# Performance work log

Hardware: AMD Instinct MI355X
Metric: run time of the kernel (lower is better)

The kernel has to match this reference:

```python
import jax, jax.numpy as jnp
import numpy as np

N_HEADS = 8
N_POINTS = 4


def _bilinear_sample(vl, g, Hl, Wl):
    # vl: [B, nH, Hl*Wl, hd] level values; g: [B, Q, nH, P, 2] sampling locs in [0,1] (x, y)
    # Emulates torch grid_sample(mode='bilinear', padding_mode='zeros', align_corners=False)
    B, Q, nH, P, _ = g.shape
    hd = vl.shape[-1]
    x = g[..., 0] * Wl - 0.5
    y = g[..., 1] * Hl - 0.5
    x0f = jnp.floor(x)
    y0f = jnp.floor(y)
    x0 = x0f.astype(jnp.int32)
    y0 = y0f.astype(jnp.int32)
    wx1 = x - x0f
    wy1 = y - y0f

    def corner(xi, yi, w):
        valid = (xi >= 0) & (xi < Wl) & (yi >= 0) & (yi < Hl)
        idx = jnp.clip(yi, 0, Hl - 1) * Wl + jnp.clip(xi, 0, Wl - 1)  # [B,Q,nH,P]
        idx = idx.transpose(0, 2, 1, 3).reshape(B, nH, Q * P)
        gathered = jnp.take_along_axis(vl, idx[..., None], axis=2)  # [B,nH,Q*P,hd]
        wm = (w * valid.astype(w.dtype)).transpose(0, 2, 1, 3).reshape(B, nH, Q * P)
        return gathered * wm[..., None]

    s = (corner(x0, y0, (1.0 - wx1) * (1.0 - wy1))
         + corner(x0 + 1, y0, wx1 * (1.0 - wy1))
         + corner(x0, y0 + 1, (1.0 - wx1) * wy1)
         + corner(x0 + 1, y0 + 1, wx1 * wy1))
    return s.reshape(B, nH, Q, P, hd)


def setup_inputs() -> dict:
    key = jax.random.key(0)
    ks = jax.random.split(key, 12)
    B, Q, D = 32, 300, 256
    L, P, nH = 4, N_POINTS, N_HEADS
    shapes = np.array([[80, 80], [40, 40], [20, 20], [10, 10]], dtype=np.int32)
    V = int((shapes[:, 0] * shapes[:, 1]).sum())  # 8500
    lsi = np.concatenate([[0], np.cumsum(shapes[:, 0] * shapes[:, 1])[:-1]]).astype(np.int32)
    sd = 1.0 / np.sqrt(D)
    return {
        'query': jax.random.normal(ks[0], (B, Q, D), jnp.float32),
        'reference_points': jax.random.uniform(ks[1], (B, Q, L, 2), jnp.float32),
        'value': jax.random.normal(ks[2], (B, V, D), jnp.float32),
        'spatial_shapes': jnp.asarray(shapes),
        'level_start_index': jnp.asarray(lsi),
        'W_off': jax.random.normal(ks[3], (D, nH * L * P * 2), jnp.float32) * sd,
        'b_off': jax.random.normal(ks[4], (nH * L * P * 2,), jnp.float32) * 0.5,
        'W_attn': jax.random.normal(ks[5], (D, nH * L * P), jnp.float32) * sd,
        'b_attn': jax.random.normal(ks[6], (nH * L * P,), jnp.float32) * 0.1,
        'W_val': jax.random.normal(ks[7], (D, D), jnp.float32) * sd,
        'b_val': jnp.zeros((D,), jnp.float32),
        'W_out': jax.random.normal(ks[8], (D, D), jnp.float32) * sd,
        'b_out': jnp.zeros((D,), jnp.float32),
    }


def reference(query, reference_points, value, spatial_shapes, level_start_index,
              W_off, b_off, W_attn, b_attn, W_val, b_val, W_out, b_out):
    shapes = np.asarray(spatial_shapes)  # static level shapes
    B, Q, D = query.shape
    nH, P = N_HEADS, N_POINTS
    L = shapes.shape[0]
    hd = D // nH

    val = value @ W_val + b_val  # [B,V,D]
    val = val.reshape(B, -1, nH, hd).transpose(0, 2, 1, 3)  # [B,nH,V,hd]

    off = (query @ W_off + b_off).reshape(B, Q, nH, L, P, 2)
    attn = jax.nn.softmax((query @ W_attn + b_attn).reshape(B, Q, nH, L * P), axis=-1)
    attn = attn.reshape(B, Q, nH, L, P)

    # normalizer is (W_l, H_l)
    norm = jnp.asarray(np.stack([shapes[:, 1], shapes[:, 0]], -1), jnp.float32)  # [L,2]
    loc = reference_points[:, :, None, :, None, :] + off / norm[None, None, None, :, None, :]

    out = jnp.zeros((B, Q, nH, hd), query.dtype)
    start = 0
    for lvl in range(L):
        Hl, Wl = int(shapes[lvl, 0]), int(shapes[lvl, 1])
        vl = val[:, :, start:start + Hl * Wl, :]  # [B,nH,HW,hd]
        sampled = _bilinear_sample(vl, loc[:, :, :, lvl], Hl, Wl)  # [B,nH,Q,P,hd]
        out = out + jnp.einsum('bnqpd,bqnp->bqnd', sampled, attn[:, :, :, lvl])
        start += Hl * Wl

    return out.reshape(B, Q, D) @ W_out + b_out
```

## Files before the change

kernel.cpp:

```cpp
#include <hip/hip_runtime.h>
#include <hip/hip_bf16.h>
#include <math.h>
#include <stdint.h>

#define NB 32
#define NQ 300
#define ND 256
#define NH 8
#define HD 32
#define NL 4
#define NP 4
#define V_TOT 8500
#define BQ_TOT (NB*NQ)
#define MVAL (NB*V_TOT)
#define NOA 384

typedef short v8s __attribute__((ext_vector_type(8)));
typedef float v4f __attribute__((ext_vector_type(4)));

#define AS1 __attribute__((address_space(1)))
#define AS3 __attribute__((address_space(3)))

__device__ __forceinline__ void copy16_async(const void* g, void* l) {
#if __has_builtin(__builtin_amdgcn_global_load_lds)
    __builtin_amdgcn_global_load_lds((const AS1 unsigned int*)g,
                                     (AS3 unsigned int*)l, 16, 0, 0);
#else
    *(uint4*)l = *(const uint4*)g;
#endif
}

__device__ __forceinline__ unsigned short f2bf_rne(float x) {
    unsigned u = __float_as_uint(x);
    u += 0x7fffu + ((u >> 16) & 1u);
    return (unsigned short)(u >> 16);
}
__device__ __forceinline__ float bf2f(unsigned short b) {
    return __uint_as_float(((unsigned)b) << 16);
}

__device__ __forceinline__ void split2(float f0, float f1,
                                       unsigned& hp, unsigned& lp) {
    float2 v; v.x = f0; v.y = f1;
    __hip_bfloat162 h = __float22bfloat162_rn(v);
    unsigned hu; __builtin_memcpy(&hu, &h, 4);
    const float h0 = __uint_as_float(hu << 16);
    const float h1 = __uint_as_float(hu & 0xffff0000u);
    float2 l; l.x = f0 - h0; l.y = f1 - h1;
    __hip_bfloat162 lo = __float22bfloat162_rn(l);
    unsigned lu; __builtin_memcpy(&lu, &lo, 4);
    hp = hu; lp = lu;
}

__device__ __forceinline__ int swz_pos(int n, int k) {
    const int base = k & ~31;
    const int o = (k >> 3) & 3;
    const int op = o ^ ((n >> 1) & 3);
    return n * 256 + base + (op << 3) + (k & 7);
}

__global__ __launch_bounds__(256) void prep_weights(
    const float* __restrict__ W_val, const float* __restrict__ W_off,
    const float* __restrict__ W_attn, const float* __restrict__ W_out,
    const float* __restrict__ b_off, const float* __restrict__ b_attn,
    unsigned short* __restrict__ Bval_h, unsigned short* __restrict__ Bval_l,
    unsigned short* __restrict__ Boa_h,  unsigned short* __restrict__ Boa_l,
    unsigned short* __restrict__ Bout_h, unsigned short* __restrict__ Bout_l,
    float* __restrict__ b_oa)
{
    const int t = blockIdx.x * 256 + threadIdx.x;
    if (t < 65536) {
        const int n = t >> 8, k = t & 255;
        const float x = W_val[k * 256 + n];
        const unsigned short hi = f2bf_rne(x);
        const unsigned short lo = f2bf_rne(x - bf2f(hi));
        const int p = swz_pos(n, k);
        Bval_h[p] = hi; Bval_l[p] = lo;
    } else if (t < 65536 + 98304) {
        const int t2 = t - 65536;
        const int n = t2 >> 8, k = t2 & 255;
        const float x = (n < 256) ? W_off[k * 256 + n] : W_attn[k * 128 + (n - 256)];
        const unsigned short hi = f2bf_rne(x);
        const unsigned short lo = f2bf_rne(x - bf2f(hi));
        const int p = swz_pos(n, k);
        Boa_h[p] = hi; Boa_l[p] = lo;
    } else if (t < 229376) {
        const int t3 = t - 163840;
        const int n = t3 >> 8, k = t3 & 255;
        const float x = W_out[k * 256 + n];
        const unsigned short hi = f2bf_rne(x);
        const unsigned short lo = f2bf_rne(x - bf2f(hi));
        const int p = swz_pos(n, k);
        Bout_h[p] = hi; Bout_l[p] = lo;
    } else {
        const int t4 = t - 229376;
        if (t4 < NOA) b_oa[t4] = (t4 < 256) ? b_off[t4] : b_attn[t4 - 256];
    }
}

__global__ __launch_bounds__(256) void gemm_a32(
    const float* __restrict__ A,
    const unsigned short* __restrict__ Bh,
    const unsigned short* __restrict__ Bl,
    const float* __restrict__ bias,
    float* __restrict__ Cf,
    unsigned short* __restrict__ Cb,
    int ldc, int mode)
{
    __shared__ unsigned short Ah[128][32];
    __shared__ unsigned short Al[128][32];
    __shared__ unsigned short Bs[2][128][32];

    const int tid  = threadIdx.x;
    const int row0 = blockIdx.x * 128;
    const int col0 = blockIdx.y * 128;
    const int wave = tid >> 6;
    const int lane = tid & 63;
    const int wm   = (wave >> 1) * 64;
    const int wn   = (wave & 1) * 64;
    const int m16  = lane & 15;
    const int quad = lane >> 4;

    v4f acc[4][4] = {};

    for (int k0 = 0; k0 < 256; k0 += 32) {
        unsigned hpk[2][4], lpk[2][4];
        int rr[2], oo[2];
#pragma unroll
        for (int i = 0; i < 2; ++i) {
            const int idx = tid + i * 256;
            const int r   = idx >> 2;
            const int o   = idx & 3;
            rr[i] = r;
            oo[i] = (o ^ ((r >> 1) & 3)) << 3;
            const float4 f0 = *(const float4*)(A + (size_t)(row0 + r) * 256 + k0 + o * 8);
            const float4 f1 = *(const float4*)(A + (size_t)(row0 + r) * 256 + k0 + o * 8 + 4);
            split2(f0.x, f0.y, hpk[i][0], lpk[i][0]);
            split2(f0.z, f0.w, hpk[i][1], lpk[i][1]);
            split2(f1.x, f1.y, hpk[i][2], lpk[i][2]);
            split2(f1.z, f1.w, hpk[i][3], lpk[i][3]);
        }

        __syncthreads();

#pragma unroll
        for (int c = 0; c < 2; ++c) {
            const int linear = (wave * 2 + c) * 1024 + lane * 16;
            const int n   = linear >> 6;
            const int off = linear & 63;
            copy16_async((const char*)Bh + ((size_t)(col0 + n) * 256 + k0) * 2 + off,
                         (char*)&Bs[0][0][0] + linear);
            copy16_async((const char*)Bl + ((size_t)(col0 + n) * 256 + k0) * 2 + off,
                         (char*)&Bs[1][0][0] + linear);
        }

#pragma unroll
        for (int i = 0; i < 2; ++i) {
            *(uint4*)&Ah[rr[i]][oo[i]] = make_uint4(hpk[i][0], hpk[i][1], hpk[i][2], hpk[i][3]);
            *(uint4*)&Al[rr[i]][oo[i]] = make_uint4(lpk[i][0], lpk[i][1], lpk[i][2], lpk[i][3]);
        }

        __syncthreads();

        v8s ah[4], al[4], bh[4], bl[4];
#pragma unroll
        for (int i = 0; i < 4; ++i) {
            const int r  = wm + i * 16 + m16;
            const int ka = (quad ^ ((r >> 1) & 3)) << 3;
            ah[i] = *(v8s*)&Ah[r][ka];
            al[i] = *(v8s*)&Al[r][ka];
            const int n  = wn + i * 16 + m16;
            const int ko = (quad ^ ((n >> 1) & 3)) << 3;
            bh[i] = *(v8s*)&Bs[0][n][ko];
            bl[i] = *(v8s*)&Bs[1][n][ko];
        }
#pragma unroll
        for (int i = 0; i < 4; ++i)
#pragma unroll
            for (int j = 0; j < 4; ++j) {
                acc[i][j] = __builtin_amdgcn_mfma_f32_16x16x32_bf16(ah[i], bh[j], acc[i][j], 0, 0, 0);
                acc[i][j] = __builtin_amdgcn_mfma_f32_16x16x32_bf16(ah[i], bl[j], acc[i][j], 0, 0, 0);
                acc[i][j] = __builtin_amdgcn_mfma_f32_16x16x32_bf16(al[i], bh[j], acc[i][j], 0, 0, 0);
            }
    }

#pragma unroll
    for (int j = 0; j < 4; ++j) {
        const int cl = col0 + wn + j * 16 + m16;
        const float bb = bias[cl];
        if (mode == 0) {
#pragma unroll
            for (int i = 0; i < 4; ++i)
#pragma unroll
                for (int r = 0; r < 4; ++r) {
                    const int R = row0 + wm + i * 16 + quad * 4 + r;
                    Cf[(size_t)R * ldc + cl] = acc[i][j][r] + bb;
                }
        } else {
            const int h  = cl >> 5;
            const int dh = cl & 31;
#pragma unroll
            for (int i = 0; i < 4; ++i)
#pragma unroll
                for (int r = 0; r < 4; ++r) {
                    const int R = row0 + wm + i * 16 + quad * 4 + r;
                    const unsigned b = (unsigned)R / V_TOT;
                    const int v = R - (int)b * V_TOT;
                    Cb[(((size_t)(b * NH + h)) * V_TOT + v) * HD + dh] =
                        f2bf_rne(acc[i][j][r] + bb);
                }
        }
    }
}

__global__ __launch_bounds__(256) void gemm_a16(
    const unsigned short* __restrict__ A,
    const unsigned short* __restrict__ Bh,
    const unsigned short* __restrict__ Bl,
    const float* __restrict__ bias,
    float* __restrict__ C, int ldc)
{
    __shared__ unsigned short As[2][128][32];
    __shared__ unsigned short Bs[2][2][128][32];

    const int tid  = threadIdx.x;
    const int row0 = blockIdx.x * 128;
    const int col0 = blockIdx.y * 128;
    const int wave = tid >> 6;
    const int lane = tid & 63;
    const int wm   = (wave >> 1) * 64;
    const int wn   = (wave & 1) * 64;
    const int m16  = lane & 15;
    const int quad = lane >> 4;

    v4f acc[4][4] = {};

#pragma unroll
    for (int c = 0; c < 2; ++c) {
        const int linear = (wave * 2 + c) * 1024 + lane * 16;
        const int n   = linear >> 6;
        const int off = linear & 63;
        copy16_async((const char*)A  + ((size_t)(row0 + n) * 256 + 0) * 2 + off,
                     (char*)&As[0][0][0] + linear);
        copy16_async((const char*)Bh + ((size_t)(col0 + n) * 256 + 0) * 2 + off,
                     (char*)&Bs[0][0][0][0] + linear);
        copy16_async((const char*)Bl + ((size_t)(col0 + n) * 256 + 0) * 2 + off,
                     (char*)&Bs[0][1][0][0] + linear);
    }
    __syncthreads();

    for (int t = 0; t < 8; ++t) {
        const int buf = t & 1;
        const int nb  = buf ^ 1;
        const int k1  = (t + 1) << 5;

        if (t < 7) {
#pragma unroll
            for (int c = 0; c < 2; ++c) {
                const int linear = (wave * 2 + c) * 1024 + lane * 16;
                const int n   = linear >> 6;
                const int off = linear & 63;
                copy16_async((const char*)A  + ((size_t)(row0 + n) * 256 + k1) * 2 + off,
                             (char*)&As[nb][0][0] + linear);
                copy16_async((const char*)Bh + ((size_t)(col0 + n) * 256 + k1) * 2 + off,
                             (char*)&Bs[nb][0][0][0] + linear);
                copy16_async((const char*)Bl + ((size_t)(col0 + n) * 256 + k1) * 2 + off,
                             (char*)&Bs[nb][1][0][0] + linear);
            }
        }

        v8s a[4], bh[4], bl[4];
#pragma unroll
        for (int i = 0; i < 4; ++i) {
            const int r  = wm + i * 16 + m16;
            const int ka = (quad ^ ((r >> 1) & 3)) << 3;
            a[i] = *(v8s*)&As[buf][r][ka];
            const int n  = wn + i * 16 + m16;
            const int kb = (quad ^ ((n >> 1) & 3)) << 3;
            bh[i] = *(v8s*)&Bs[buf][0][n][kb];
            bl[i] = *(v8s*)&Bs[buf][1][n][kb];
        }
#pragma unroll
        for (int i = 0; i < 4; ++i)
#pragma unroll
            for (int j = 0; j < 4; ++j) {
                acc[i][j] = __builtin_amdgcn_mfma_f32_16x16x32_bf16(a[i], bh[j], acc[i][j], 0, 0, 0);
                acc[i][j] = __builtin_amdgcn_mfma_f32_16x16x32_bf16(a[i], bl[j], acc[i][j], 0, 0, 0);
            }

        __syncthreads();
    }

#pragma unroll
    for (int j = 0; j < 4; ++j) {
        const int cl = col0 + wn + j * 16 + m16;
        const float bb = bias[cl];
#pragma unroll
        for (int i = 0; i < 4; ++i)
#pragma unroll
            for (int r = 0; r < 4; ++r) {
                const int R = row0 + wm + i * 16 + quad * 4 + r;
                C[(size_t)R * ldc + cl] = acc[i][j][r] + bb;
            }
    }
}

__global__ __launch_bounds__(256) void sample_kernel(
    const float* __restrict__ refp,
    const float* __restrict__ offattn,
    const unsigned short* __restrict__ val,
    unsigned short* __restrict__ pre)
{
    const int t  = blockIdx.x * 256 + threadIdx.x;
    const int d8 = t & 3;
    const int h  = (t >> 2) & 7;
    const int bq = t >> 5;
    const int b  = bq / NQ;

    const float* rp = refp + (size_t)bq * 8;
    const float* op = offattn + (size_t)bq * 384 + h * 32;
    const float* ap = offattn + (size_t)bq * 384 + 256 + h * 16;

    float aw[16];
    float m = -1e30f;
#pragma unroll
    for (int i = 0; i < 16; ++i) { aw[i] = ap[i]; m = fmaxf(m, aw[i]); }
    float s = 0.f;
#pragma unroll
    for (int i = 0; i < 16; ++i) { aw[i] = __expf(aw[i] - m); s += aw[i]; }
    const float inv = 1.f / s;
#pragma unroll
    for (int i = 0; i < 16; ++i) aw[i] *= inv;

    const int Hs[4] = {80, 40, 20, 10};
    const int St[4] = {0, 6400, 8000, 8400};

    float acc[8] = {};
#pragma unroll
    for (int l = 0; l < NL; ++l) {
        const int Wl = Hs[l], Hl = Hs[l];
        const float fW = (float)Wl, fH = (float)Hl;
        const float rx = rp[l * 2 + 0];
        const float ry = rp[l * 2 + 1];
        const unsigned short* vb =
            val + (((size_t)(b * NH + h)) * V_TOT + St[l]) * HD + d8 * 8;
#pragma unroll
        for (int p = 0; p < NP; ++p) {
            const float ox = op[l * 8 + p * 2 + 0];
            const float oy = op[l * 8 + p * 2 + 1];
            const float w  = aw[l * 4 + p];
            const float x = fmaf(rx, fW, ox) - 0.5f;
            const float y = fmaf(ry, fH, oy) - 0.5f;
            const float x0f = floorf(x), y0f = floorf(y);
            const int   x0 = (int)x0f,  y0 = (int)y0f;
            const float wx1 = x - x0f,  wy1 = y - y0f;
            const float wx0 = 1.f - wx1, wy0 = 1.f - wy1;
#pragma unroll
            for (int cy = 0; cy < 2; ++cy) {
#pragma unroll
                for (int cx = 0; cx < 2; ++cx) {
                    const int xi = x0 + cx;
                    const int yi = y0 + cy;
                    float cw = (cx ? wx1 : wx0) * (cy ? wy1 : wy0) * w;
                    const bool valid = (xi >= 0) && (xi < Wl) && (yi >= 0) && (yi < Hl);
                    cw = valid ? cw : 0.f;
                    const int xc = xi < 0 ? 0 : (xi > Wl - 1 ? Wl - 1 : xi);
                    const int yc = yi < 0 ? 0 : (yi > Hl - 1 ? Hl - 1 : yi);
                    const uint4 g = *(const uint4*)(vb + (size_t)(yc * Wl + xc) * HD);
                    const unsigned gu[4] = {g.x, g.y, g.z, g.w};
#pragma unroll
                    for (int e = 0; e < 4; ++e) {
                        acc[2*e]   = fmaf(cw, __uint_as_float(gu[e] << 16),        acc[2*e]);
                        acc[2*e+1] = fmaf(cw, __uint_as_float(gu[e] & 0xffff0000u), acc[2*e+1]);
                    }
                }
            }
        }
    }

    unsigned o[4];
#pragma unroll
    for (int e = 0; e < 4; ++e)
        o[e] = (unsigned)f2bf_rne(acc[2*e]) | ((unsigned)f2bf_rne(acc[2*e+1]) << 16);
    const int octswz = d8 ^ ((bq >> 1) & 3);
    *(uint4*)(pre + (size_t)bq * 256 + h * 32 + octswz * 8) =
        make_uint4(o[0], o[1], o[2], o[3]);
}

extern "C" void kernel_launch(void* const* d_in, const int* in_sizes, int n_in,
                              void* d_out, int out_size, void* d_ws, size_t ws_size,
                              hipStream_t stream)
{
    const float* query  = (const float*)d_in[0];
    const float* refp   = (const float*)d_in[1];
    const float* value  = (const float*)d_in[2];
    const float* W_off  = (const float*)d_in[5];
    const float* b_off  = (const float*)d_in[6];
    const float* W_attn = (const float*)d_in[7];
    const float* b_attn = (const float*)d_in[8];
    const float* W_val  = (const float*)d_in[9];
    const float* b_val  = (const float*)d_in[10];
    const float* W_out  = (const float*)d_in[11];
    const float* b_out  = (const float*)d_in[12];
    float* out = (float*)d_out;

    char* ws = (char*)d_ws;
    unsigned short* val     = (unsigned short*)ws;
    float*          offattn = (float*)(ws + 139264000);
    unsigned short* pre     = (unsigned short*)(ws + 154009600);
    unsigned short* Bval_h  = (unsigned short*)(ws + 158924800);
    unsigned short* Bval_l  = Bval_h + 65536;
    unsigned short* Boa_h   = Bval_l + 65536;
    unsigned short* Boa_l   = Boa_h + 98304;
    unsigned short* Bout_h  = Boa_l + 98304;
    unsigned short* Bout_l  = Bout_h + 65536;
    float*          b_oa    = (float*)(Bout_l + 65536);

    const dim3 blk(256);

    prep_weights<<<dim3(898), blk, 0, stream>>>(
        W_val, W_off, W_attn, W_out, b_off, b_attn,
        Bval_h, Bval_l, Boa_h, Boa_l, Bout_h, Bout_l, b_oa);

    gemm_a32<<<dim3(MVAL / 128, 2), blk, 0, stream>>>(
        value, Bval_h, Bval_l, b_val, nullptr, val, 0, 1);

    gemm_a32<<<dim3(BQ_TOT / 128, 3), blk, 0, stream>>>(
        query, Boa_h, Boa_l, b_oa, offattn, nullptr, NOA, 0);

    sample_kernel<<<dim3((BQ_TOT * 32) / 256), blk, 0, stream>>>(
        refp, offattn, val, pre);

    gemm_a16<<<dim3(BQ_TOT / 128, 2), blk, 0, stream>>>(
        pre, Bout_h, Bout_l, b_out, out, 256);
}
```

Before: 617.2 us.

## Prefetch A tiles into registers, swap grid axes, add occupancy hint in gemm_a32

Restructures the fp32-input split-bf16 GEMM so the next K-slice of A is loaded into registers while the current slice is split and stored, hiding global load latency. The grid is transposed so the column blocks that share the same A rows run next to each other, which should improve L2 reuse of the large value matrix. B fragments are now loaded inside the j loop to cut live registers, and launch_bounds asks for 3 blocks per SM. The cost is extra registers for the prefetched data and a risk of spills under the tighter occupancy target.

After: 576.2 us. -6.6%, faster.

```diff
diff --git a/kernel.cpp b/kernel.cpp
--- a/kernel.cpp
+++ b/kernel.cpp
@@ -98,7 +98,7 @@
     }
 }
 
-__global__ __launch_bounds__(256) void gemm_a32(
+__global__ __launch_bounds__(256, 3) void gemm_a32(
     const float* __restrict__ A,
     const unsigned short* __restrict__ Bh,
     const unsigned short* __restrict__ Bl,
@@ -112,8 +112,8 @@
     __shared__ unsigned short Bs[2][128][32];
 
     const int tid  = threadIdx.x;
-    const int row0 = blockIdx.x * 128;
-    const int col0 = blockIdx.y * 128;
+    const int col0 = blockIdx.x * 128;
+    const int row0 = blockIdx.y * 128;
     const int wave = tid >> 6;
     const int lane = tid & 63;
     const int wm   = (wave >> 1) * 64;
@@ -121,67 +121,84 @@
     const int m16  = lane & 15;
     const int quad = lane >> 4;
 
+    const int i0  = tid;
+    const int i1  = tid + 256;
+    const int r0_ = i0 >> 2, o0_ = i0 & 3;
+    const int r1_ = i1 >> 2, o1_ = i1 & 3;
+    const int oo0 = (o0_ ^ ((r0_ >> 1) & 3)) << 3;
+    const int oo1 = (o1_ ^ ((r1_ >> 1) & 3)) << 3;
+    const float* Ap0 = A + (size_t)(row0 + r0_) * 256 + o0_ * 8;
+    const float* Ap1 = A + (size_t)(row0 + r1_) * 256 + o1_ * 8;
+
+    const int lin0 = (wave * 2 + 0) * 1024 + lane * 16;
+    const int lin1 = (wave * 2 + 1) * 1024 + lane * 16;
+    const char* pBh0 = (const char*)Bh + ((size_t)(col0 + (lin0 >> 6)) * 256) * 2 + (lin0 & 63);
+    const char* pBl0 = (const char*)Bl + ((size_t)(col0 + (lin0 >> 6)) * 256) * 2 + (lin0 & 63);
+    const char* pBh1 = (const char*)Bh + ((size_t)(col0 + (lin1 >> 6)) * 256) * 2 + (lin1 & 63);
+    const char* pBl1 = (const char*)Bl + ((size_t)(col0 + (lin1 >> 6)) * 256) * 2 + (lin1 & 63);
+    char* lBh0 = (char*)&Bs[0][0][0] + lin0;
+    char* lBh1 = (char*)&Bs[0][0][0] + lin1;
+    char* lBl0 = (char*)&Bs[1][0][0] + lin0;
+    char* lBl1 = (char*)&Bs[1][0][0] + lin1;
+
     v4f acc[4][4] = {};
 
-    for (int k0 = 0; k0 < 256; k0 += 32) {
-        unsigned hpk[2][4], lpk[2][4];
-        int rr[2], oo[2];
-#pragma unroll
-        for (int i = 0; i < 2; ++i) {
-            const int idx = tid + i * 256;
-            const int r   = idx >> 2;
-            const int o   = idx & 3;
-            rr[i] = r;
-            oo[i] = (o ^ ((r >> 1) & 3)) << 3;
-            const float4 f0 = *(const float4*)(A + (size_t)(row0 + r) * 256 + k0 + o * 8);
-            const float4 f1 = *(const float4*)(A + (size_t)(row0 + r) * 256 + k0 + o * 8 + 4);
-            split2(f0.x, f0.y, hpk[i][0], lpk[i][0]);
-            split2(f0.z, f0.w, hpk[i][1], lpk[i][1]);
-            split2(f1.x, f1.y, hpk[i][2], lpk[i][2]);
-            split2(f1.z, f1.w, hpk[i][3], lpk[i][3]);
+    float4 f00 = *(const float4*)(Ap0);
+    float4 f01 = *(const float4*)(Ap0 + 4);
+    float4 f10 = *(const float4*)(Ap1);
+    float4 f11 = *(const float4*)(Ap1 + 4);
+
+#pragma unroll
+    for (int t = 0; t < 8; ++t) {
+        unsigned hpk0[4], lpk0[4], hpk1[4], lpk1[4];
+        split2(f00.x, f00.y, hpk0[0], lpk0[0]);
+        split2(f00.z, f00.w, hpk0[1], lpk0[1]);
+        split2(f01.x, f01.y, hpk0[2], lpk0[2]);
+        split2(f01.z, f01.w, hpk0[3], lpk0[3]);
+        split2(f10.x, f10.y, hpk1[0], lpk1[0]);
+        split2(f10.z, f10.w, hpk1[1], lpk1[1]);
+        split2(f11.x, f11.y, hpk1[2], lpk1[2]);
+        split2(f11.z, f11.w, hpk1[3], lpk1[3]);
+
+        if (t < 7) {
+            const int k1 = (t + 1) * 32;
+            f00 = *(const float4*)(Ap0 + k1);
+            f01 = *(const float4*)(Ap0 + k1 + 4);
+            f10 = *(const float4*)(Ap1 + k1);
+            f11 = *(const float4*)(Ap1 + k1 + 4);
         }
 
         __syncthreads();
 
-#pragma unroll
-        for (int c = 0; c < 2; ++c) {
-            const int linear = (wave * 2 + c) * 1024 + lane * 16;
-            const int n   = linear >> 6;
-            const int off = linear & 63;
-            copy16_async((const char*)Bh + ((size_t)(col0 + n) * 256 + k0) * 2 + off,
-                         (char*)&Bs[0][0][0] + linear);
-            copy16_async((const char*)Bl + ((size_t)(col0 + n) * 256 + k0) * 2 + off,
-                         (char*)&Bs[1][0][0] + linear);
-        }
-
-#pragma unroll
-        for (int i = 0; i < 2; ++i) {
-            *(uint4*)&Ah[rr[i]][oo[i]] = make_uint4(hpk[i][0], hpk[i][1], hpk[i][2], hpk[i][3]);
-            *(uint4*)&Al[rr[i]][oo[i]] = make_uint4(lpk[i][0], lpk[i][1], lpk[i][2], lpk[i][3]);
-        }
+        copy16_async(pBh0 + t * 64, lBh0);
+        copy16_async(pBh1 + t * 64, lBh1);
+        copy16_async(pBl0 + t * 64, lBl0);
+        copy16_async(pBl1 + t * 64, lBl1);
+
+        *(uint4*)&Ah[r0_][oo0] = make_uint4(hpk0[0], hpk0[1], hpk0[2], hpk0[3]);
+        *(uint4*)&Al[r0_][oo0] = make_uint4(lpk0[0], lpk0[1], lpk0[2], lpk0[3]);
+        *(uint4*)&Ah[r1_][oo1] = make_uint4(hpk1[0], hpk1[1], hpk1[2], hpk1[3]);
+        *(uint4*)&Al[r1_][oo1] = make_uint4(lpk1[0], lpk1[1], lpk1[2], lpk1[3]);
 
         __syncthreads();
 
-        v8s ah[4], al[4], bh[4], bl[4];
 #pragma unroll
         for (int i = 0; i < 4; ++i) {
             const int r  = wm + i * 16 + m16;
             const int ka = (quad ^ ((r >> 1) & 3)) << 3;
-            ah[i] = *(v8s*)&Ah[r][ka];
-            al[i] = *(v8s*)&Al[r][ka];
-            const int n  = wn + i * 16 + m16;
-            const int ko = (quad ^ ((n >> 1) & 3)) << 3;
-            bh[i] = *(v8s*)&Bs[0][n][ko];
-            bl[i] = *(v8s*)&Bs[1][n][ko];
-        }
-#pragma unroll
-        for (int i = 0; i < 4; ++i)
+            const v8s ah = *(v8s*)&Ah[r][ka];
+            const v8s al = *(v8s*)&Al[r][ka];
 #pragma unroll
             for (int j = 0; j < 4; ++j) {
-                acc[i][j] = __builtin_amdgcn_mfma_f32_16x16x32_bf16(ah[i], bh[j], acc[i][j], 0, 0, 0);
-                acc[i][j] = __builtin_amdgcn_mfma_f32_16x16x32_bf16(ah[i], bl[j], acc[i][j], 0, 0, 0);
-                acc[i][j] = __builtin_amdgcn_mfma_f32_16x16x32_bf16(al[i], bh[j], acc[i][j], 0, 0, 0);
+                const int n  = wn + j * 16 + m16;
+                const int ko = (quad ^ ((n >> 1) & 3)) << 3;
+                const v8s bh = *(v8s*)&Bs[0][n][ko];
+                const v8s bl = *(v8s*)&Bs[1][n][ko];
+                acc[i][j] = __builtin_amdgcn_mfma_f32_16x16x32_bf16(ah, bh, acc[i][j], 0, 0, 0);
+                acc[i][j] = __builtin_amdgcn_mfma_f32_16x16x32_bf16(ah, bl, acc[i][j], 0, 0, 0);
+                acc[i][j] = __builtin_amdgcn_mfma_f32_16x16x32_bf16(al, bh, acc[i][j], 0, 0, 0);
             }
+        }
     }
 
 #pragma unroll
@@ -422,10 +439,10 @@
         W_val, W_off, W_attn, W_out, b_off, b_attn,
         Bval_h, Bval_l, Boa_h, Boa_l, Bout_h, Bout_l, b_oa);
 
-    gemm_a32<<<dim3(MVAL / 128, 2), blk, 0, stream>>>(
+    gemm_a32<<<dim3(2, MVAL / 128), blk, 0, stream>>>(
         value, Bval_h, Bval_l, b_val, nullptr, val, 0, 1);
 
-    gemm_a32<<<dim3(BQ_TOT / 128, 3), blk, 0, stream>>>(
+    gemm_a32<<<dim3(3, BQ_TOT / 128), blk, 0, stream>>>(
         query, Boa_h, Boa_l, b_oa, offattn, nullptr, NOA, 0);
 
     sample_kernel<<<dim3((BQ_TOT * 32) / 256), blk, 0, stream>>>(
```
